# Kernel tuning notes

Hardware: AMD Instinct MI355X
Metric: run time of the kernel (lower is better)

Reference implementation:

```python
import jax, jax.numpy as jnp
import numpy as np

B, T, D, W, H = 8, 2048, 1024, 16, 8
HD = D // H  # head dim = 128
EPS = 1e-5


def _layernorm(x, g, b):
    m = jnp.mean(x, axis=-1, keepdims=True)
    v = jnp.var(x, axis=-1, keepdims=True)
    return (x - m) / jnp.sqrt(v + EPS) * g + b


def setup_inputs() -> dict:
    key = jax.random.key(0)
    ks = jax.random.split(key, 8)
    s = 0.02
    return {
        "frame_features": jax.random.normal(ks[0], (B, T, D), dtype=jnp.float32),
        "frame_indices": jnp.arange(B * T, dtype=jnp.int64).reshape(B, T),
        # nn.MultiheadAttention packed in-projection (3D, D) and out projection
        "w_qkv": jax.random.normal(ks[1], (3 * D, D), dtype=jnp.float32) * s,
        "b_qkv": jnp.zeros((3 * D,), dtype=jnp.float32),
        "w_out": jax.random.normal(ks[2], (D, D), dtype=jnp.float32) * s,
        "b_out": jnp.zeros((D,), dtype=jnp.float32),
        # FFN: Linear(D, 4D) -> GELU -> Linear(4D, D)
        "w1": jax.random.normal(ks[3], (4 * D, D), dtype=jnp.float32) * s,
        "b1": jnp.zeros((4 * D,), dtype=jnp.float32),
        "w2": jax.random.normal(ks[4], (D, 4 * D), dtype=jnp.float32) * s,
        "b2": jnp.zeros((D,), dtype=jnp.float32),
        "g1": jnp.ones((D,), dtype=jnp.float32),
        "beta1": jnp.zeros((D,), dtype=jnp.float32),
        "g2": jnp.ones((D,), dtype=jnp.float32),
        "beta2": jnp.zeros((D,), dtype=jnp.float32),
    }


def _forward(frame_features, frame_indices, w_qkv, b_qkv, w_out, b_out,
             w1, b1, w2, b2, g1, beta1, g2, beta2):
    # --- sinusoidal temporal positional encoding, indexed by frame number ---
    pos = frame_indices.astype(jnp.float32)[..., None]          # (B, T, 1)
    div = jnp.exp(-jnp.log(10000.0) * jnp.arange(0, D, 2, dtype=jnp.float32) / D)
    ang = pos * div                                              # (B, T, D/2)
    pe = jnp.stack([jnp.sin(ang), jnp.cos(ang)], axis=-1).reshape(B, T, D)
    x = frame_features + pe

    # --- block-diagonal (local window) attention, all windows in one pass ---
    nw = T // W
    xw = x.reshape(B, nw, W, D)
    qkv = jnp.einsum('bnwd,ed->bnwe', xw, w_qkv) + b_qkv         # (B, nw, W, 3D)
    q, k, v = jnp.split(qkv, 3, axis=-1)
    q = q.reshape(B, nw, W, H, HD)
    k = k.reshape(B, nw, W, H, HD)
    v = v.reshape(B, nw, W, H, HD)
    scores = jnp.einsum('bnqhd,bnkhd->bnhqk', q, k) / jnp.sqrt(jnp.float32(HD))
    attn = jax.nn.softmax(scores, axis=-1)
    o = jnp.einsum('bnhqk,bnkhd->bnqhd', attn, v).reshape(B, nw, W, D)
    attn_out = jnp.einsum('bnwd,ed->bnwe', o, w_out) + b_out

    h = _layernorm(xw + attn_out, g1, beta1)
    ffn = jnp.einsum('bnwf,df->bnwd', jax.nn.gelu(
        jnp.einsum('bnwd,fd->bnwf', h, w1) + b1, approximate=False), w2) + b2
    out = _layernorm(h + ffn, g2, beta2)
    return out.reshape(B, T, D)


def reference(frame_features, frame_indices, w_qkv, b_qkv, w_out, b_out,
              w1, b1, w2, b2, g1, beta1, g2, beta2):
    return _forward(frame_features, frame_indices, w_qkv, b_qkv, w_out, b_out,
                    w1, b1, w2, b2, g1, beta1, g2, beta2)
```

## Files before the change

kernel.cpp:

```cpp
#include <hip/hip_runtime.h>
#include <math.h>

typedef __bf16 bf16;
typedef __bf16 bf16x8 __attribute__((ext_vector_type(8)));
typedef __bf16 bf16x4 __attribute__((ext_vector_type(4)));
typedef __bf16 bf16x2 __attribute__((ext_vector_type(2)));
typedef float f32x4 __attribute__((ext_vector_type(4)));

#define ROWS 16384

typedef __attribute__((address_space(3))) void* lds_vp;
typedef const __attribute__((address_space(1))) void* glb_vp;
typedef __attribute__((address_space(3))) bf16 lbf16;
__device__ __forceinline__ void gload16(const void* g, void* l) {
  __builtin_amdgcn_global_load_lds((glb_vp)g, (lds_vp)l, 16, 0, 0);
}

template<int OFF>
__device__ __forceinline__ bf16x8 dsr(uint32_t a) {
  bf16x8 r;
  asm volatile("ds_read_b128 %0, %1 offset:%2" : "=v"(r) : "v"(a), "n"(OFF));
  return r;
}

__global__ __launch_bounds__(256) void cast_kernel(
    const float* __restrict__ src, bf16* __restrict__ dst, int n)
{
  int i = (blockIdx.x * 256 + threadIdx.x) * 8;
  if (i >= n) return;
  float4 a = *(const float4*)(src + i);
  float4 b = *(const float4*)(src + i + 4);
  bf16x8 o;
  o[0] = (bf16)a.x; o[1] = (bf16)a.y; o[2] = (bf16)a.z; o[3] = (bf16)a.w;
  o[4] = (bf16)b.x; o[5] = (bf16)b.y; o[6] = (bf16)b.z; o[7] = (bf16)b.w;
  *(bf16x8*)(dst + i) = o;
}

__global__ __launch_bounds__(256) void pe_add_kernel(
    const float* __restrict__ ff, const int* __restrict__ idx, bf16* __restrict__ x)
{
  int p   = blockIdx.x * 256 + threadIdx.x;
  int row = p >> 9;
  int j   = p & 511;
  float pos = (float)idx[row];
  float d2  = (float)(2 * j) * (1.0f / 1024.0f);
  float dv  = expf(-9.210340371976184f * d2);
  float ang = pos * dv;
  float s, c;
  sincosf(ang, &s, &c);
  int base = row * 1024 + 2 * j;
  float2 f = *(const float2*)(ff + base);
  bf16x2 o;
  o[0] = (bf16)(f.x + s);
  o[1] = (bf16)(f.y + c);
  *(bf16x2*)(x + base) = o;
}

#define MFMA16 __builtin_amdgcn_mfma_f32_16x16x32_bf16

template<bool GELU, bool RES>
__global__ __launch_bounds__(512, 2) void gemm8(
    const bf16* __restrict__ A, const bf16* __restrict__ Bw,
    const float* __restrict__ bias, const bf16* __restrict__ resid,
    bf16* __restrict__ C, int M, int N, int K)
{
  extern __shared__ char smem[];

  const int tid  = threadIdx.x;
  const int wave = tid >> 6;
  const int lane = tid & 63;
  const int wm = wave >> 2, wn = wave & 3;
  const int ln = lane & 15, q = lane >> 4;
  const int wm8 = wm * 8, wn4 = wn * 4;

  const int nwg = gridDim.x;
  const int nbn = N >> 8;
  const int swz = (blockIdx.x & 7) * (nwg >> 3) + (blockIdx.x >> 3);
  const int bm = (swz / nbn) << 8;
  const int bn = (swz % nbn) << 8;

  const uint32_t lbase = (uint32_t)(size_t)(lbf16*)smem;
  const uint32_t rswb  = (uint32_t)((ln * 64 + q * 16) ^ (((ln >> 3) & 1) << 5));
  const uint32_t rA01 = lbase + wm8 * 1024 + rswb;
  const uint32_t rA23 = rA01 + 65536;
  const uint32_t rB01 = lbase + 16384 + wn4 * 1024 + rswb;
  const uint32_t rB23 = rB01 + 65536;

  const int le = lane ^ (((lane >> 5) & 1) << 1);
  const int sr = le >> 2;
  const int sc = (le & 3) * 8;
  const bf16* gAw = A  + (size_t)(bm + wave * 32 + sr) * K + sc;
  const bf16* gBw = Bw + (size_t)(bn + wave * 32 + sr) * K + sc;

#define STAGE_A(BB, KOFF) do { \
    char* _d = smem + (BB) * 32768 + wave * 2048; \
    gload16(gAw + (KOFF), _d); \
    gload16(gAw + 16 * (size_t)K + (KOFF), _d + 1024); } while (0)
#define STAGE_B(BB, KOFF) do { \
    char* _d = smem + (BB) * 32768 + 16384 + wave * 2048; \
    gload16(gBw + (KOFF), _d); \
    gload16(gBw + 16 * (size_t)K + (KOFF), _d + 1024); } while (0)

  f32x4 acc[8][4];
#pragma unroll
  for (int i = 0; i < 8; i++)
#pragma unroll
    for (int j = 0; j < 4; j++) acc[i][j] = {0.f, 0.f, 0.f, 0.f};

  const int nkt = K >> 5;

  STAGE_A(0, 0);  STAGE_B(0, 0);
  STAGE_A(1, 32); STAGE_B(1, 32);
  STAGE_A(2, 64); STAGE_B(2, 64);
  asm volatile("s_waitcnt vmcnt(8)");
  __builtin_amdgcn_s_barrier();

  bf16x8 a0, a1, a2, a3, a4, a5, a6, a7, b0, b1, b2, b3;

#define MF4(T, AT) \
    acc[T][0] = MFMA16(AT, b0, acc[T][0], 0, 0, 0); \
    acc[T][1] = MFMA16(AT, b1, acc[T][1], 0, 0, 0); \
    acc[T][2] = MFMA16(AT, b2, acc[T][2], 0, 0, 0); \
    acc[T][3] = MFMA16(AT, b3, acc[T][3], 0, 0, 0);

#define PH1(BB, M) { \
    const uint32_t _ra = (BB) < 2 ? rA01 : rA23; \
    const uint32_t _rb = (BB) < 2 ? rB01 : rB23; \
    a0 = dsr<(((BB) & 1) * 32768) + 0>(_ra); \
    a1 = dsr<(((BB) & 1) * 32768) + 1024>(_ra); \
    a2 = dsr<(((BB) & 1) * 32768) + 2048>(_ra); \
    a3 = dsr<(((BB) & 1) * 32768) + 3072>(_ra); \
    b0 = dsr<(((BB) & 1) * 32768) + 0>(_rb); \
    b1 = dsr<(((BB) & 1) * 32768) + 1024>(_rb); \
    b2 = dsr<(((BB) & 1) * 32768) + 2048>(_rb); \
    b3 = dsr<(((BB) & 1) * 32768) + 3072>(_rb); \
    if ((M) + 3 < nkt) STAGE_A((((BB) + 3) & 3), ((M) + 3) * 32); \
    __builtin_amdgcn_s_barrier(); \
    asm volatile("s_waitcnt lgkmcnt(0)"); \
    __builtin_amdgcn_sched_barrier(0); \
    __builtin_amdgcn_s_setprio(1); \
    MF4(0, a0) MF4(1, a1) MF4(2, a2) MF4(3, a3) \
    __builtin_amdgcn_s_setprio(0); \
    __builtin_amdgcn_sched_barrier(0); \
  }

#define PH2(BB, M) { \
    const uint32_t _ra = (BB) < 2 ? rA01 : rA23; \
    a4 = dsr<(((BB) & 1) * 32768) + 4096>(_ra); \
    a5 = dsr<(((BB) & 1) * 32768) + 5120>(_ra); \
    a6 = dsr<(((BB) & 1) * 32768) + 6144>(_ra); \
    a7 = dsr<(((BB) & 1) * 32768) + 7168>(_ra); \
    if ((M) + 3 < nkt) STAGE_B((((BB) + 3) & 3), ((M) + 3) * 32); \
    asm volatile("s_waitcnt lgkmcnt(0)"); \
    __builtin_amdgcn_sched_barrier(0); \
    __builtin_amdgcn_s_setprio(1); \
    MF4(4, a4) MF4(5, a5) MF4(6, a6) MF4(7, a7) \
    __builtin_amdgcn_s_setprio(0); \
    __builtin_amdgcn_sched_barrier(0); \
    if ((M) < nkt - 3)       { asm volatile("s_waitcnt vmcnt(8)"); } \
    else if ((M) == nkt - 3) { asm volatile("s_waitcnt vmcnt(4)"); } \
    else if ((M) == nkt - 2) { asm volatile("s_waitcnt vmcnt(0)"); } \
    __builtin_amdgcn_s_barrier(); \
  }

  for (int mm = 0; mm < nkt; mm += 4) {
    PH1(0, mm)     PH2(0, mm)
    PH1(1, mm + 1) PH2(1, mm + 1)
    PH1(2, mm + 2) PH2(2, mm + 2)
    PH1(3, mm + 3) PH2(3, mm + 3)
  }
#undef PH1
#undef PH2
#undef MF4
#undef STAGE_A
#undef STAGE_B

  float bv[4];
#pragma unroll
  for (int tn = 0; tn < 4; tn++) bv[tn] = bias[bn + wn * 64 + tn * 16 + ln];
  bf16* eb = (bf16*)smem;
  const int lrow = tid >> 4;
  const int cb   = (tid & 15) * 16;
#pragma unroll
  for (int tm = 0; tm < 8; tm++) {
    __syncthreads();
#pragma unroll
    for (int tn = 0; tn < 4; tn++)
#pragma unroll
      for (int i = 0; i < 4; i++)
        eb[(wm * 16 + q * 4 + i) * 264 + wn * 64 + tn * 16 + ln] =
            (bf16)(acc[tm][tn][i] + bv[tn]);
    __syncthreads();
    int gR = bm + (lrow >> 4) * 128 + tm * 16 + (lrow & 15);
    size_t rowoff = (size_t)gR * N + bn + cb;
    bf16x8 v0 = *(const bf16x8*)&eb[lrow * 264 + cb];
    bf16x8 v1 = *(const bf16x8*)&eb[lrow * 264 + cb + 8];
    if (RES) {
      bf16x8 r0 = *(const bf16x8*)(resid + rowoff);
      bf16x8 r1 = *(const bf16x8*)(resid + rowoff + 8);
#pragma unroll
      for (int u = 0; u < 8; u++) {
        v0[u] = (bf16)((float)v0[u] + (float)r0[u]);
        v1[u] = (bf16)((float)v1[u] + (float)r1[u]);
      }
    }
    if (GELU) {
#pragma unroll
      for (int u = 0; u < 8; u++) {
        float a = (float)v0[u], c = (float)v1[u];
        float ea = __builtin_amdgcn_exp2f(2.3022082f * a * (1.0f + 0.044715f * a * a));
        float ec = __builtin_amdgcn_exp2f(2.3022082f * c * (1.0f + 0.044715f * c * c));
        v0[u] = (bf16)(a - a * __builtin_amdgcn_rcpf(ea + 1.0f));
        v1[u] = (bf16)(c - c * __builtin_amdgcn_rcpf(ec + 1.0f));
      }
    }
    *(bf16x8*)(C + rowoff)     = v0;
    *(bf16x8*)(C + rowoff + 8) = v1;
  }
}

__global__ __launch_bounds__(256) void attn_kernel(
    const bf16* __restrict__ qkv, bf16* __restrict__ o)
{
  __shared__ float sq[16][132], sk[16][132], sv[16][132];
  __shared__ float ss[16][17];

  int wid = blockIdx.x;
  int h   = wid & 7;
  int win = wid >> 3;
  int tb  = win * 16;

  int t  = threadIdx.x;
  int r  = t >> 4;
  int c8 = (t & 15) * 8;

  const bf16* base = qkv + (size_t)(tb + r) * 3072 + c8;
  bf16x8 qv = *(const bf16x8*)(base + h * 128);
  bf16x8 kv = *(const bf16x8*)(base + 1024 + h * 128);
  bf16x8 vv = *(const bf16x8*)(base + 2048 + h * 128);
#pragma unroll
  for (int u = 0; u < 8; u++) {
    sq[r][c8 + u] = (float)qv[u];
    sk[r][c8 + u] = (float)kv[u];
    sv[r][c8 + u] = (float)vv[u];
  }
  __syncthreads();

  {
    int i = t >> 4, jj = t & 15;
    float s = 0.f;
#pragma unroll 8
    for (int d = 0; d < 128; d++) s += sq[i][d] * sk[jj][d];
    ss[i][jj] = s * 0.08838834764831845f;
  }
  __syncthreads();

  if (t < 16) {
    float m = -1e30f;
    for (int jj = 0; jj < 16; jj++) m = fmaxf(m, ss[t][jj]);
    float sum = 0.f;
    for (int jj = 0; jj < 16; jj++) { float e = expf(ss[t][jj] - m); ss[t][jj] = e; sum += e; }
    float inv = 1.0f / sum;
    for (int jj = 0; jj < 16; jj++) ss[t][jj] *= inv;
  }
  __syncthreads();

  {
    int i = t >> 4; int d0 = (t & 15) * 8;
    float acc[8] = {0, 0, 0, 0, 0, 0, 0, 0};
#pragma unroll
    for (int jj = 0; jj < 16; jj++) {
      float a = ss[i][jj];
#pragma unroll
      for (int u = 0; u < 8; u++) acc[u] += a * sv[jj][d0 + u];
    }
    bf16* op = o + (size_t)(tb + i) * 1024 + h * 128 + d0;
#pragma unroll
    for (int u = 0; u < 8; u++) op[u] = (bf16)acc[u];
  }
}

template<typename OUT_T>
__global__ __launch_bounds__(256) void ln_kernel(
    const bf16* __restrict__ x, const float* __restrict__ g,
    const float* __restrict__ b, OUT_T* __restrict__ y)
{
  __shared__ float red[8];
  int row = blockIdx.x;
  int t   = threadIdx.x;
  int lane = t & 63, wave = t >> 6;

  bf16x4 v4 = *(const bf16x4*)(x + (size_t)row * 1024 + t * 4);
  float v[4];
  float s = 0.f, sq = 0.f;
#pragma unroll
  for (int u = 0; u < 4; u++) {
    v[u] = (float)v4[u];
    s += v[u];
    sq += v[u] * v[u];
  }
  for (int off = 32; off > 0; off >>= 1) {
    s  += __shfl_down(s, off);
    sq += __shfl_down(sq, off);
  }
  if (lane == 0) { red[wave * 2] = s; red[wave * 2 + 1] = sq; }
  __syncthreads();
  float st = red[0] + red[2] + red[4] + red[6];
  float qt = red[1] + red[3] + red[5] + red[7];
  float mean = st * (1.0f / 1024.0f);
  float var  = qt * (1.0f / 1024.0f) - mean * mean;
  float inv  = rsqrtf(var + 1e-5f);
  int c = t * 4;
  OUT_T* yr = y + (size_t)row * 1024 + c;
#pragma unroll
  for (int u = 0; u < 4; u++)
    yr[u] = (OUT_T)((v[u] - mean) * inv * g[c + u] + b[c + u]);
}

extern "C" void kernel_launch(void* const* d_in, const int* in_sizes, int n_in,
                              void* d_out, int out_size, void* d_ws, size_t ws_size,
                              hipStream_t stream) {
  const float* ff    = (const float*)d_in[0];
  const int*   idx   = (const int*)d_in[1];
  const float* w_qkv = (const float*)d_in[2];
  const float* b_qkv = (const float*)d_in[3];
  const float* w_out = (const float*)d_in[4];
  const float* b_out = (const float*)d_in[5];
  const float* w1    = (const float*)d_in[6];
  const float* b1    = (const float*)d_in[7];
  const float* w2    = (const float*)d_in[8];
  const float* b2    = (const float*)d_in[9];
  const float* g1    = (const float*)d_in[10];
  const float* be1   = (const float*)d_in[11];
  const float* g2    = (const float*)d_in[12];
  const float* be2   = (const float*)d_in[13];
  float* out = (float*)d_out;

  static bool attrs_done = false;
  if (!attrs_done) {
    attrs_done = true;
    hipFuncSetAttribute(reinterpret_cast<const void*>(&gemm8<false, false>),
                        hipFuncAttributeMaxDynamicSharedMemorySize, 131072);
    hipFuncSetAttribute(reinterpret_cast<const void*>(&gemm8<false, true>),
                        hipFuncAttributeMaxDynamicSharedMemorySize, 131072);
    hipFuncSetAttribute(reinterpret_cast<const void*>(&gemm8<true, false>),
                        hipFuncAttributeMaxDynamicSharedMemorySize, 131072);
  }

  char* p = (char*)d_ws;
  bf16* x_bf = (bf16*)p;  p += (size_t)ROWS * 1024 * 2;
  bf16* big  = (bf16*)p;  p += (size_t)ROWS * 4096 * 2;
  bf16* s_bf = (bf16*)p;  p += (size_t)ROWS * 1024 * 2;
  bf16* h_bf = (bf16*)p;  p += (size_t)ROWS * 1024 * 2;
  bf16* wqb  = (bf16*)p;  p += (size_t)3072 * 1024 * 2;
  bf16* wob  = (bf16*)p;  p += (size_t)1024 * 1024 * 2;
  bf16* w1b  = (bf16*)p;  p += (size_t)4096 * 1024 * 2;
  bf16* w2b  = (bf16*)p;  p += (size_t)1024 * 4096 * 2;
  bf16* o_bf = big + (size_t)ROWS * 3072;
  bf16* g_bf = big;

  cast_kernel<<<3072 * 1024 / 8 / 256, 256, 0, stream>>>(w_qkv, wqb, 3072 * 1024);
  cast_kernel<<<1024 * 1024 / 8 / 256, 256, 0, stream>>>(w_out, wob, 1024 * 1024);
  cast_kernel<<<4096 * 1024 / 8 / 256, 256, 0, stream>>>(w1, w1b, 4096 * 1024);
  cast_kernel<<<1024 * 4096 / 8 / 256, 256, 0, stream>>>(w2, w2b, 1024 * 4096);

  pe_add_kernel<<<ROWS * 512 / 256, 256, 0, stream>>>(ff, idx, x_bf);

  gemm8<false, false><<<64 * 12, 512, 131072, stream>>>(
      x_bf, wqb, b_qkv, nullptr, big, ROWS, 3072, 1024);
  attn_kernel<<<(ROWS / 16) * 8, 256, 0, stream>>>(big, o_bf);
  gemm8<false, true><<<64 * 4, 512, 131072, stream>>>(
      o_bf, wob, b_out, x_bf, s_bf, ROWS, 1024, 1024);
  ln_kernel<bf16><<<ROWS, 256, 0, stream>>>(s_bf, g1, be1, h_bf);
  gemm8<true, false><<<64 * 16, 512, 131072, stream>>>(
      h_bf, w1b, b1, nullptr, big, ROWS, 4096, 1024);
  gemm8<false, true><<<64 * 4, 512, 131072, stream>>>(
      g_bf, w2b, b2, h_bf, s_bf, ROWS, 1024, 4096);
  ln_kernel<float><<<ROWS, 256, 0, stream>>>(s_bf, g2, be2, out);
}
```

Measured before the change: 676.8 us.

## Collapse two-phase GEMM k-loop into single-phase tiles with compiler LDS reads

```diff
diff --git a/kernel.cpp b/kernel.cpp
--- a/kernel.cpp
+++ b/kernel.cpp
@@ -11,16 +11,8 @@
 
 typedef __attribute__((address_space(3))) void* lds_vp;
 typedef const __attribute__((address_space(1))) void* glb_vp;
-typedef __attribute__((address_space(3))) bf16 lbf16;
 __device__ __forceinline__ void gload16(const void* g, void* l) {
   __builtin_amdgcn_global_load_lds((glb_vp)g, (lds_vp)l, 16, 0, 0);
-}
-
-template<int OFF>
-__device__ __forceinline__ bf16x8 dsr(uint32_t a) {
-  bf16x8 r;
-  asm volatile("ds_read_b128 %0, %1 offset:%2" : "=v"(r) : "v"(a), "n"(OFF));
-  return r;
 }
 
 __global__ __launch_bounds__(256) void cast_kernel(
@@ -79,12 +71,10 @@
   const int bm = (swz / nbn) << 8;
   const int bn = (swz % nbn) << 8;
 
-  const uint32_t lbase = (uint32_t)(size_t)(lbf16*)smem;
-  const uint32_t rswb  = (uint32_t)((ln * 64 + q * 16) ^ (((ln >> 3) & 1) << 5));
-  const uint32_t rA01 = lbase + wm8 * 1024 + rswb;
-  const uint32_t rA23 = rA01 + 65536;
-  const uint32_t rB01 = lbase + 16384 + wn4 * 1024 + rswb;
-  const uint32_t rB23 = rB01 + 65536;
+  const bf16* lA = (const bf16*)smem;
+  const int rsw = (ln * 32 + q * 8) ^ (((ln >> 3) & 1) << 4);
+  const int raw = wm8 * 512 + rsw;
+  const int rbw = 8192 + wn4 * 512 + rsw;
 
   const int le = lane ^ (((lane >> 5) & 1) << 1);
   const int sr = le >> 2;
@@ -107,6 +97,10 @@
 #pragma unroll
     for (int j = 0; j < 4; j++) acc[i][j] = {0.f, 0.f, 0.f, 0.f};
 
+  float bv[4];
+#pragma unroll
+  for (int tn = 0; tn < 4; tn++) bv[tn] = bias[bn + wn * 64 + tn * 16 + ln];
+
   const int nkt = K >> 5;
 
   STAGE_A(0, 0);  STAGE_B(0, 0);
@@ -115,69 +109,60 @@
   asm volatile("s_waitcnt vmcnt(8)");
   __builtin_amdgcn_s_barrier();
 
-  bf16x8 a0, a1, a2, a3, a4, a5, a6, a7, b0, b1, b2, b3;
-
-#define MF4(T, AT) \
-    acc[T][0] = MFMA16(AT, b0, acc[T][0], 0, 0, 0); \
-    acc[T][1] = MFMA16(AT, b1, acc[T][1], 0, 0, 0); \
-    acc[T][2] = MFMA16(AT, b2, acc[T][2], 0, 0, 0); \
-    acc[T][3] = MFMA16(AT, b3, acc[T][3], 0, 0, 0);
-
-#define PH1(BB, M) { \
-    const uint32_t _ra = (BB) < 2 ? rA01 : rA23; \
-    const uint32_t _rb = (BB) < 2 ? rB01 : rB23; \
-    a0 = dsr<(((BB) & 1) * 32768) + 0>(_ra); \
-    a1 = dsr<(((BB) & 1) * 32768) + 1024>(_ra); \
-    a2 = dsr<(((BB) & 1) * 32768) + 2048>(_ra); \
-    a3 = dsr<(((BB) & 1) * 32768) + 3072>(_ra); \
-    b0 = dsr<(((BB) & 1) * 32768) + 0>(_rb); \
-    b1 = dsr<(((BB) & 1) * 32768) + 1024>(_rb); \
-    b2 = dsr<(((BB) & 1) * 32768) + 2048>(_rb); \
-    b3 = dsr<(((BB) & 1) * 32768) + 3072>(_rb); \
-    if ((M) + 3 < nkt) STAGE_A((((BB) + 3) & 3), ((M) + 3) * 32); \
-    __builtin_amdgcn_s_barrier(); \
-    asm volatile("s_waitcnt lgkmcnt(0)"); \
-    __builtin_amdgcn_sched_barrier(0); \
+#define MFROW(T, AF) \
+    acc[T][0] = MFMA16(AF, bf0, acc[T][0], 0, 0, 0); \
+    acc[T][1] = MFMA16(AF, bf1, acc[T][1], 0, 0, 0); \
+    acc[T][2] = MFMA16(AF, bf2, acc[T][2], 0, 0, 0); \
+    acc[T][3] = MFMA16(AF, bf3, acc[T][3], 0, 0, 0);
+
+#define KT(B_, KST, STG, VMS) { \
+    if (STG) { STAGE_A((((B_) + 3) & 3), (KST)); STAGE_B((((B_) + 3) & 3), (KST)); } \
+    const bf16* _pa = lA + (B_) * 16384 + raw; \
+    const bf16* _pb = lA + (B_) * 16384 + rbw; \
+    bf16x8 af0 = *(const bf16x8*)(_pa); \
+    bf16x8 af1 = *(const bf16x8*)(_pa + 512); \
+    bf16x8 af2 = *(const bf16x8*)(_pa + 1024); \
+    bf16x8 af3 = *(const bf16x8*)(_pa + 1536); \
+    bf16x8 af4 = *(const bf16x8*)(_pa + 2048); \
+    bf16x8 af5 = *(const bf16x8*)(_pa + 2560); \
+    bf16x8 af6 = *(const bf16x8*)(_pa + 3072); \
+    bf16x8 af7 = *(const bf16x8*)(_pa + 3584); \
+    bf16x8 bf0 = *(const bf16x8*)(_pb); \
+    bf16x8 bf1 = *(const bf16x8*)(_pb + 512); \
+    bf16x8 bf2 = *(const bf16x8*)(_pb + 1024); \
+    bf16x8 bf3 = *(const bf16x8*)(_pb + 1536); \
     __builtin_amdgcn_s_setprio(1); \
-    MF4(0, a0) MF4(1, a1) MF4(2, a2) MF4(3, a3) \
+    MFROW(0, af0) MFROW(1, af1) MFROW(2, af2) MFROW(3, af3) \
+    MFROW(4, af4) MFROW(5, af5) MFROW(6, af6) MFROW(7, af7) \
     __builtin_amdgcn_s_setprio(0); \
-    __builtin_amdgcn_sched_barrier(0); \
-  }
-
-#define PH2(BB, M) { \
-    const uint32_t _ra = (BB) < 2 ? rA01 : rA23; \
-    a4 = dsr<(((BB) & 1) * 32768) + 4096>(_ra); \
-    a5 = dsr<(((BB) & 1) * 32768) + 5120>(_ra); \
-    a6 = dsr<(((BB) & 1) * 32768) + 6144>(_ra); \
-    a7 = dsr<(((BB) & 1) * 32768) + 7168>(_ra); \
-    if ((M) + 3 < nkt) STAGE_B((((BB) + 3) & 3), ((M) + 3) * 32); \
-    asm volatile("s_waitcnt lgkmcnt(0)"); \
-    __builtin_amdgcn_sched_barrier(0); \
-    __builtin_amdgcn_s_setprio(1); \
-    MF4(4, a4) MF4(5, a5) MF4(6, a6) MF4(7, a7) \
-    __builtin_amdgcn_s_setprio(0); \
-    __builtin_amdgcn_sched_barrier(0); \
-    if ((M) < nkt - 3)       { asm volatile("s_waitcnt vmcnt(8)"); } \
-    else if ((M) == nkt - 3) { asm volatile("s_waitcnt vmcnt(4)"); } \
-    else if ((M) == nkt - 2) { asm volatile("s_waitcnt vmcnt(0)"); } \
-    __builtin_amdgcn_s_barrier(); \
-  }
-
-  for (int mm = 0; mm < nkt; mm += 4) {
-    PH1(0, mm)     PH2(0, mm)
-    PH1(1, mm + 1) PH2(1, mm + 1)
-    PH1(2, mm + 2) PH2(2, mm + 2)
-    PH1(3, mm + 3) PH2(3, mm + 3)
-  }
-#undef PH1
-#undef PH2
-#undef MF4
+    VMS; \
+    __builtin_amdgcn_s_barrier(); }
+
+#define V8 asm volatile("s_waitcnt vmcnt(8)")
+#define V4 asm volatile("s_waitcnt vmcnt(4)")
+#define V0 asm volatile("s_waitcnt vmcnt(0)")
+#define VN (void)0
+
+  for (int mm = 0; mm < nkt - 4; mm += 4) {
+    const int kst = (mm + 3) * 32;
+    KT(0, kst,       true, V8)
+    KT(1, kst + 32,  true, V8)
+    KT(2, kst + 64,  true, V8)
+    KT(3, kst + 96,  true, V8)
+  }
+  KT(0, (nkt - 1) * 32, true,  V8)
+  KT(1, 0,              false, V4)
+  KT(2, 0,              false, V0)
+  KT(3, 0,              false, VN)
+#undef KT
+#undef MFROW
+#undef V8
+#undef V4
+#undef V0
+#undef VN
 #undef STAGE_A
 #undef STAGE_B
 
-  float bv[4];
-#pragma unroll
-  for (int tn = 0; tn < 4; tn++) bv[tn] = bias[bn + wn * 64 + tn * 16 + ln];
   bf16* eb = (bf16*)smem;
   const int lrow = tid >> 4;
   const int cb   = (tid & 15) * 16;
```

Result: no change. 668.9 us (-1.2%).
